# Performance work log

Measured on AMD Instinct MI355X. Metric: run time of the kernel, lower is better.

The kernel has to match this reference:

```python
import jax, jax.numpy as jnp
import numpy as np

N_NODES = 100000
N_EDGES = 1200000
D = 64
NUM_LAYERS = 3
K = 3


def setup_inputs() -> dict:
    key = jax.random.key(0)
    k1, k2, k3, k4 = jax.random.split(key, 4)
    x = jax.random.normal(k1, (N_NODES, D), dtype=jnp.float32)
    edge_index = jax.random.randint(k2, (2, N_EDGES), 0, N_NODES, dtype=jnp.int64)
    # per-layer Chebyshev linear weights [L, K, in, out] and single bias per layer [L, out]
    W = jax.random.normal(k3, (NUM_LAYERS, K, D, D), dtype=jnp.float32) / np.sqrt(D)
    b = jax.random.normal(k4, (NUM_LAYERS, D), dtype=jnp.float32) * 0.01
    return {"x": x, "edge_index": edge_index, "W": W, "b": b}


def _cheb_norm(edge_index, n_nodes):
    # PyG ChebConv.__norm__ with sym normalization, lambda_max=2.0, no edge weights:
    # scaled Laplacian L_hat = -D^{-1/2} A D^{-1/2} (diagonal cancels to 0).
    row, col = edge_index[0], edge_index[1]
    deg = jax.ops.segment_sum(jnp.ones_like(row, dtype=jnp.float32), row,
                              num_segments=n_nodes)
    deg_inv_sqrt = jnp.where(deg > 0, jax.lax.rsqrt(jnp.maximum(deg, 1.0)), 0.0)
    norm = -deg_inv_sqrt[row] * deg_inv_sqrt[col]  # [E]
    return norm


def _propagate(h, src, dst, norm, n_nodes):
    # out[i] = sum_{e: dst_e = i} norm_e * h[src_e]
    msgs = norm[:, None] * h[src]  # [E, D]
    return jax.ops.segment_sum(msgs, dst, num_segments=n_nodes)


def _cheb_conv(h, src, dst, norm, Wl, bl, n_nodes):
    # Tx_0 = h; Tx_1 = L_hat h; Tx_k = 2 L_hat Tx_{k-1} - Tx_{k-2}
    Tx0 = h
    out = Tx0 @ Wl[0]
    Tx1 = _propagate(Tx0, src, dst, norm, n_nodes)
    out = out + Tx1 @ Wl[1]
    for k in range(2, K):
        Tx2 = 2.0 * _propagate(Tx1, src, dst, norm, n_nodes) - Tx0
        out = out + Tx2 @ Wl[k]
        Tx0, Tx1 = Tx1, Tx2
    return out + bl


def reference(x, edge_index, W, b) -> jnp.ndarray:
    n_nodes = x.shape[0]
    src, dst = edge_index[0], edge_index[1]  # flow source_to_target: j=src, i=dst
    norm = _cheb_norm(edge_index, n_nodes)
    # input_dim == hidden_dim -> no input projection; h_prev starts as x
    h_prev = x
    for i in range(NUM_LAYERS):
        inp = x if i == 0 else h_prev
        out = _cheb_conv(inp, src, dst, norm, W[i], b[i], n_nodes)
        if i > 0:
            out = out + h_prev
        h_prev = jax.nn.relu(out)  # dropout identity in eval mode
    return h_prev
```

## Files before the change

### kernel.cpp

```cpp
#include <hip/hip_runtime.h>

#define N_NODES 100000
#define N_EDGES 1200000
#define D 64
#define NUM_LAYERS 3

#define NB 196
#define BSZ 512
#define NPAD (NB * BSZ)
#define CHUNK 4096
#define NCHUNK ((N_EDGES + CHUNK - 1) / CHUNK)
#define ZROW N_NODES
#define BSLACK 3592
#define CAP 8192

typedef unsigned int uint;
typedef unsigned short u16;

using short8 = __attribute__((ext_vector_type(8))) short;
using f32x4  = __attribute__((ext_vector_type(4))) float;

static __device__ __forceinline__ float b2f(u16 u) {
    return __uint_as_float(((uint)u) << 16);
}
static __device__ __forceinline__ u16 f2b(float f) {
    uint u = __float_as_uint(f);
    return (u16)((u + 0x7FFFu + ((u >> 16) & 1u)) >> 16);
}

__global__ __launch_bounds__(256) void part_kernel(const int* __restrict__ src,
        const int* __restrict__ dst, int* __restrict__ cursD, int* __restrict__ cursS,
        int* __restrict__ dstPart, u16* __restrict__ srcPart, int E) {
    __shared__ int eS[CHUNK], eT[CHUNK];
    __shared__ int hD[NB], hS[NB], bD[NB], bS[NB];
    int e0 = blockIdx.x * CHUNK;
    int n = min(CHUNK, E - e0);
    for (int i = threadIdx.x; i < NB; i += 256) { hD[i] = 0; hS[i] = 0; }
    for (int i = threadIdx.x; i < n; i += 256) { eS[i] = src[e0 + i]; eT[i] = dst[e0 + i]; }
    __syncthreads();
    for (int i = threadIdx.x; i < n; i += 256) {
        atomicAdd(&hD[((unsigned)eT[i]) >> 9], 1);
        atomicAdd(&hS[((unsigned)eS[i]) >> 9], 1);
    }
    __syncthreads();
    for (int i = threadIdx.x; i < NB; i += 256) {
        bD[i] = hD[i] ? atomicAdd(&cursD[i], hD[i]) : 0;
        bS[i] = hS[i] ? atomicAdd(&cursS[i], hS[i]) : 0;
        hD[i] = 0; hS[i] = 0;
    }
    __syncthreads();
    for (int i = threadIdx.x; i < n; i += 256) {
        int s = eS[i], t = eT[i];
        int kb = ((unsigned)t) >> 9;
        int pos = bD[kb] + atomicAdd(&hD[kb], 1);
        if (pos < (kb + 1) * CAP) dstPart[pos] = ((t & 511) << 20) | s;
        kb = ((unsigned)s) >> 9;
        pos = bS[kb] + atomicAdd(&hS[kb], 1);
        if (pos < (kb + 1) * CAP) srcPart[pos] = (u16)(s & 511);
    }
}

__global__ __launch_bounds__(256) void csr_kernel(const int* __restrict__ cursD,
        const int* __restrict__ dstPart, int* __restrict__ rowptr,
        int* __restrict__ rowend, int* __restrict__ cv) {
    __shared__ int cnt[BSZ], curs[BSZ], psum[256];
    int b = blockIdx.x, t = threadIdx.x;
    int node0 = b * BSZ;
    int eb = b * CAP;
    int ee = min(cursD[b], (b + 1) * CAP);
    int padbase = eb + b * BSLACK;
    for (int i = t; i < BSZ; i += 256) cnt[i] = 0;
    __syncthreads();
    for (int e = eb + t; e < ee; e += 256)
        atomicAdd(&cnt[((unsigned)dstPart[e]) >> 20], 1);
    __syncthreads();
    int c0 = cnt[2 * t], c1 = cnt[2 * t + 1];
    int p0 = (c0 + 7) & ~7, p1 = (c1 + 7) & ~7;
    psum[t] = p0 + p1;
    __syncthreads();
    for (int off = 1; off < 256; off <<= 1) {
        int u = (t >= off) ? psum[t - off] : 0;
        __syncthreads();
        psum[t] += u;
        __syncthreads();
    }
    int excl = psum[t] - p0 - p1;
    int start0 = padbase + excl;
    int start1 = start0 + p0;
    curs[2 * t] = start0;
    curs[2 * t + 1] = start1;
    int n0 = node0 + 2 * t;
    if (n0 < N_NODES)     { rowptr[n0]     = start0; rowend[n0]     = start0 + p0; }
    if (n0 + 1 < N_NODES) { rowptr[n0 + 1] = start1; rowend[n0 + 1] = start1 + p1; }
    __syncthreads();
    for (int e = eb + t; e < ee; e += 256) {
        int p = dstPart[e];
        int loc = ((unsigned)p) >> 20;
        int pos = atomicAdd(&curs[loc], 1);
        cv[pos] = p & 0xFFFFF;
    }
    __syncthreads();
    for (int q = c0; q < p0; ++q) cv[start0 + q] = ZROW;
    for (int q = c1; q < p1; ++q) cv[start1 + q] = ZROW;
}

__global__ __launch_bounds__(256) void degs_kernel(const int* __restrict__ cursS,
        const u16* __restrict__ srcPart, float* __restrict__ sArr,
        float* __restrict__ rsArr, float* __restrict__ mArr) {
    __shared__ int cnt[BSZ];
    int b = blockIdx.x, t = threadIdx.x;
    int eb = b * CAP;
    int ee = min(cursS[b], (b + 1) * CAP);
    for (int i = t; i < BSZ; i += 256) cnt[i] = 0;
    __syncthreads();
    for (int e = eb + t; e < ee; e += 256)
        atomicAdd(&cnt[srcPart[e]], 1);
    __syncthreads();
    for (int i = t; i < BSZ; i += 256) {
        int node = b * BSZ + i;
        if (node < N_NODES) {
            int d = cnt[i];
            float fd = (float)d;
            sArr[node]  = (d > 0) ? rsqrtf(fd) : 1.0f;
            rsArr[node] = (d > 0) ? sqrtf(fd) : 1.0f;
            mArr[node]  = (d > 0) ? (-1.0f / fd) : 0.0f;
        }
    }
}

__global__ __launch_bounds__(256) void wprep_kernel(const float* __restrict__ W,
        u16* __restrict__ Wb, int* __restrict__ curs2,
        u16* __restrict__ za, u16* __restrict__ zb, u16* __restrict__ zc) {
    if (blockIdx.x == 0) {
        for (int k = threadIdx.x; k < 2 * NB; k += 256)
            curs2[k] = (k < NB ? k : k - NB) * CAP;
        if (threadIdx.x < 192) {
            u16* buf = (threadIdx.x < 64) ? za : (threadIdx.x < 128) ? zb : zc;
            buf[(size_t)ZROW * D + (threadIdx.x & 63)] = 0;
        }
    }
    int i = blockIdx.x * 256 + threadIdx.x;
    if (i >= 72 * 512) return;
    int j = i & 7;
    int lane = (i >> 3) & 63;
    int fid = i >> 9;
    int ni = fid & 1;
    int t = fid >> 1;
    int kt = t % 6;
    int t2 = t / 6;
    int wn = t2 & 1;
    int l = t2 >> 1;
    int k = kt * 32 + (lane >> 4) * 8 + j;
    int col = wn * 32 + ni * 16 + (lane & 15);
    float v = W[((size_t)l * 192 + k) * 64 + col];
    if (l > 0 && k == col) v += 1.0f;
    Wb[i] = f2b(v);
}

__global__ __launch_bounds__(256) void cvt_kernel(const float* __restrict__ x,
        const float* __restrict__ sArr, u16* __restrict__ g0, int nvec) {
    int i = blockIdx.x * blockDim.x + threadIdx.x;
    if (i >= nvec) return;
    float4 v = ((const float4*)x)[i];
    float dv = sArr[i >> 4];
    uint2 b;
    b.x = (uint)f2b(v.x * dv) | ((uint)f2b(v.y * dv) << 16);
    b.y = (uint)f2b(v.z * dv) | ((uint)f2b(v.w * dv) << 16);
    ((uint2*)g0)[i] = b;
}

static __device__ __forceinline__ float gather_one(const int* __restrict__ cv,
        const u16* __restrict__ g, int lane, int p, int pe) {
    float a0 = 0.f, a1 = 0.f, a2 = 0.f, a3 = 0.f,
          a4 = 0.f, a5 = 0.f, a6 = 0.f, a7 = 0.f;
    if (pe - p == 16) {
        int4 c0 = *(const int4*)(cv + p);
        int4 c1 = *(const int4*)(cv + p + 4);
        int4 c2 = *(const int4*)(cv + p + 8);
        int4 c3 = *(const int4*)(cv + p + 12);
        float v0  = b2f(g[(size_t)c0.x * D + lane]);
        float v1  = b2f(g[(size_t)c0.y * D + lane]);
        float v2  = b2f(g[(size_t)c0.z * D + lane]);
        float v3  = b2f(g[(size_t)c0.w * D + lane]);
        float v4  = b2f(g[(size_t)c1.x * D + lane]);
        float v5  = b2f(g[(size_t)c1.y * D + lane]);
        float v6  = b2f(g[(size_t)c1.z * D + lane]);
        float v7  = b2f(g[(size_t)c1.w * D + lane]);
        float v8  = b2f(g[(size_t)c2.x * D + lane]);
        float v9  = b2f(g[(size_t)c2.y * D + lane]);
        float v10 = b2f(g[(size_t)c2.z * D + lane]);
        float v11 = b2f(g[(size_t)c2.w * D + lane]);
        float v12 = b2f(g[(size_t)c3.x * D + lane]);
        float v13 = b2f(g[(size_t)c3.y * D + lane]);
        float v14 = b2f(g[(size_t)c3.z * D + lane]);
        float v15 = b2f(g[(size_t)c3.w * D + lane]);
        a0 = (v0 + v8);  a1 = (v1 + v9);  a2 = (v2 + v10); a3 = (v3 + v11);
        a4 = (v4 + v12); a5 = (v5 + v13); a6 = (v6 + v14); a7 = (v7 + v15);
    } else if (pe > p) {
        int4 ca = *(const int4*)(cv + p);
        int4 cb = *(const int4*)(cv + p + 4);
        for (;;) {
            int np = p + 8;
            bool more = np < pe;
            int4 na, nb;
            if (more) {
                na = *(const int4*)(cv + np);
                nb = *(const int4*)(cv + np + 4);
            }
            a0 += b2f(g[(size_t)ca.x * D + lane]);
            a1 += b2f(g[(size_t)ca.y * D + lane]);
            a2 += b2f(g[(size_t)ca.z * D + lane]);
            a3 += b2f(g[(size_t)ca.w * D + lane]);
            a4 += b2f(g[(size_t)cb.x * D + lane]);
            a5 += b2f(g[(size_t)cb.y * D + lane]);
            a6 += b2f(g[(size_t)cb.z * D + lane]);
            a7 += b2f(g[(size_t)cb.w * D + lane]);
            if (!more) break;
            ca = na; cb = nb; p = np;
        }
    }
    return ((a0 + a1) + (a2 + a3)) + ((a4 + a5) + (a6 + a7));
}

__global__ __launch_bounds__(256) void gather_kernel(const int* __restrict__ rowptr,
        const int* __restrict__ rowend, const int* __restrict__ cv,
        const u16* __restrict__ g, const float* __restrict__ mArr,
        u16* __restrict__ outg, int n) {
    int lane = threadIdx.x & 63;
    int nA = __builtin_amdgcn_readfirstlane((int)(blockIdx.x * 8) + ((threadIdx.x >> 6) << 1));
    if (nA >= n) return;
    const int nB = nA + 1;
    const bool hasB = nB < n;
    int p1 = rowptr[nA], pe1 = rowend[nA];
    int p2 = p1, pe2 = p1;
    if (hasB) { p2 = rowptr[nB]; pe2 = rowend[nB]; }
    float sumA, sumB = 0.0f;

    if ((pe1 - p1 == 16) && (pe2 - p2 == 16)) {
        int4 a0 = *(const int4*)(cv + p1);
        int4 a1 = *(const int4*)(cv + p1 + 4);
        int4 a2 = *(const int4*)(cv + p1 + 8);
        int4 a3 = *(const int4*)(cv + p1 + 12);
        int4 b0 = *(const int4*)(cv + p2);
        int4 b1 = *(const int4*)(cv + p2 + 4);
        int4 b2 = *(const int4*)(cv + p2 + 8);
        int4 b3 = *(const int4*)(cv + p2 + 12);
        float uA0  = b2f(g[(size_t)a0.x * D + lane]);
        float uA1  = b2f(g[(size_t)a0.y * D + lane]);
        float uA2  = b2f(g[(size_t)a0.z * D + lane]);
        float uA3  = b2f(g[(size_t)a0.w * D + lane]);
        float uA4  = b2f(g[(size_t)a1.x * D + lane]);
        float uA5  = b2f(g[(size_t)a1.y * D + lane]);
        float uA6  = b2f(g[(size_t)a1.z * D + lane]);
        float uA7  = b2f(g[(size_t)a1.w * D + lane]);
        float uA8  = b2f(g[(size_t)a2.x * D + lane]);
        float uA9  = b2f(g[(size_t)a2.y * D + lane]);
        float uA10 = b2f(g[(size_t)a2.z * D + lane]);
        float uA11 = b2f(g[(size_t)a2.w * D + lane]);
        float uA12 = b2f(g[(size_t)a3.x * D + lane]);
        float uA13 = b2f(g[(size_t)a3.y * D + lane]);
        float uA14 = b2f(g[(size_t)a3.z * D + lane]);
        float uA15 = b2f(g[(size_t)a3.w * D + lane]);
        float uB0  = b2f(g[(size_t)b0.x * D + lane]);
        float uB1  = b2f(g[(size_t)b0.y * D + lane]);
        float uB2  = b2f(g[(size_t)b0.z * D + lane]);
        float uB3  = b2f(g[(size_t)b0.w * D + lane]);
        float uB4  = b2f(g[(size_t)b1.x * D + lane]);
        float uB5  = b2f(g[(size_t)b1.y * D + lane]);
        float uB6  = b2f(g[(size_t)b1.z * D + lane]);
        float uB7  = b2f(g[(size_t)b1.w * D + lane]);
        float uB8  = b2f(g[(size_t)b2.x * D + lane]);
        float uB9  = b2f(g[(size_t)b2.y * D + lane]);
        float uB10 = b2f(g[(size_t)b2.z * D + lane]);
        float uB11 = b2f(g[(size_t)b2.w * D + lane]);
        float uB12 = b2f(g[(size_t)b3.x * D + lane]);
        float uB13 = b2f(g[(size_t)b3.y * D + lane]);
        float uB14 = b2f(g[(size_t)b3.z * D + lane]);
        float uB15 = b2f(g[(size_t)b3.w * D + lane]);
        sumA = (((uA0 + uA8) + (uA1 + uA9)) + ((uA2 + uA10) + (uA3 + uA11)))
             + (((uA4 + uA12) + (uA5 + uA13)) + ((uA6 + uA14) + (uA7 + uA15)));
        sumB = (((uB0 + uB8) + (uB1 + uB9)) + ((uB2 + uB10) + (uB3 + uB11)))
             + (((uB4 + uB12) + (uB5 + uB13)) + ((uB6 + uB14) + (uB7 + uB15)));
    } else {
        sumA = gather_one(cv, g, lane, p1, pe1);
        sumB = gather_one(cv, g, lane, p2, pe2);
    }

    outg[(size_t)nA * D + lane] = f2b(mArr[nA] * sumA);
    if (hasB)
        outg[(size_t)nB * D + lane] = f2b(mArr[nB] * sumB);
}

__global__ __launch_bounds__(256) void cheb_mfma_kernel(
        const u16* __restrict__ gin, const u16* __restrict__ gt1,
        const u16* __restrict__ gt2, const u16* __restrict__ Wbl,
        const float* __restrict__ bias, const float* __restrict__ rsArr,
        const float* __restrict__ sArr,
        u16* __restrict__ outg, float* __restrict__ outf, int last) {
    const int tid = threadIdx.x;
    const int lane = tid & 63;
    const int w = tid >> 6;
    const int wm = w & 1, wn = w >> 1;
    const int l15 = lane & 15;
    const int l4 = lane >> 4;
    const int koff = l4 * 8;

    const int mbase = blockIdx.x * 64 + wm * 32;
    const int nbase = wn * 32;

    short8 Bf[6][2];
#pragma unroll
    for (int kt = 0; kt < 6; ++kt)
#pragma unroll
        for (int ni = 0; ni < 2; ++ni)
            Bf[kt][ni] = *(const short8*)(Wbl + (size_t)(((wn * 6 + kt) * 2) + ni) * 512 + lane * 8);

    short8 G[2][2], T1[2][2], T2[2][2];
#pragma unroll
    for (int mi = 0; mi < 2; ++mi) {
        int row = mbase + mi * 16 + l15;
#pragma unroll
        for (int half = 0; half < 2; ++half) {
            size_t off = (size_t)row * 64 + half * 32 + koff;
            G[mi][half]  = *(const short8*)(gin + off);
            T1[mi][half] = *(const short8*)(gt1 + off);
            T2[mi][half] = *(const short8*)(gt2 + off);
        }
    }

    float bj0 = bias[nbase + l15];
    float bj1 = bias[nbase + 16 + l15];

    f32x4 acc[2][2];
#pragma unroll
    for (int mi = 0; mi < 2; ++mi)
#pragma unroll
        for (int ni = 0; ni < 2; ++ni)
#pragma unroll
            for (int r = 0; r < 4; ++r) acc[mi][ni][r] = 0.0f;

#pragma unroll
    for (int kt = 0; kt < 6; ++kt) {
        short8 Af[2];
#pragma unroll
        for (int mi = 0; mi < 2; ++mi) {
            short8 a;
            if (kt < 2) {
                a = G[mi][kt];
            } else if (kt < 4) {
                a = T1[mi][kt - 2];
            } else {
                short8 a2 = T2[mi][kt - 4];
                short8 ai = G[mi][kt - 4];
#pragma unroll
                for (int j = 0; j < 8; ++j)
                    a[j] = (short)f2b(fmaf(2.0f, b2f((u16)a2[j]), -b2f((u16)ai[j])));
            }
            Af[mi] = a;
        }
#pragma unroll
        for (int mi = 0; mi < 2; ++mi)
#pragma unroll
            for (int ni = 0; ni < 2; ++ni)
                acc[mi][ni] = __builtin_amdgcn_mfma_f32_16x16x32_bf16(
                    Af[mi], Bf[kt][ni], acc[mi][ni], 0, 0, 0);
    }

    float4 rsv[2], sv[2];
#pragma unroll
    for (int mi = 0; mi < 2; ++mi) {
        rsv[mi] = *(const float4*)(rsArr + mbase + mi * 16 + l4 * 4);
        if (!last) sv[mi] = *(const float4*)(sArr + mbase + mi * 16 + l4 * 4);
    }
#pragma unroll
    for (int mi = 0; mi < 2; ++mi)
#pragma unroll
        for (int r = 0; r < 4; ++r) {
            int node = mbase + mi * 16 + l4 * 4 + r;
            if (node >= N_NODES) continue;
            float rsr = ((const float*)&rsv[mi])[r];
#pragma unroll
            for (int ni = 0; ni < 2; ++ni) {
                int col = nbase + ni * 16 + l15;
                size_t o = (size_t)node * 64 + col;
                float v = fmaf(rsr, acc[mi][ni][r], (ni ? bj1 : bj0));
                v = fmaxf(v, 0.0f);
                if (last) {
                    outf[o] = v;
                } else {
                    float sr = ((const float*)&sv[mi])[r];
                    outg[o] = f2b(v * sr);
                }
            }
        }
}

extern "C" void kernel_launch(void* const* d_in, const int* in_sizes, int n_in,
                              void* d_out, int out_size, void* d_ws, size_t ws_size,
                              hipStream_t stream) {
    const float* x = (const float*)d_in[0];
    const int* ei = (const int*)d_in[1];
    const float* W = (const float*)d_in[2];
    const float* b = (const float*)d_in[3];
    float* out = (float*)d_out;

    const int* src = ei;
    const int* dst = ei + N_EDGES;

    const size_t NDP = (size_t)NPAD * D;
    const size_t CVSZ = (size_t)NB * (CAP + BSLACK) + 64;

    char* w = (char*)d_ws;
    int*   curs2  = (int*)w;        w += (size_t)512 * 4;
    int*   rowptr = (int*)w;        w += (size_t)NPAD * 4;
    int*   rowend = (int*)w;        w += (size_t)NPAD * 4;
    float* sArr   = (float*)w;      w += (size_t)NPAD * 4;
    float* rsArr  = (float*)w;      w += (size_t)NPAD * 4;
    float* mArr   = (float*)w;      w += (size_t)NPAD * 4;
    u16*   Wb     = (u16*)w;        w += (size_t)72 * 512 * 2;
    int*   cv     = (int*)w;        w += ((CVSZ + 63) & ~(size_t)63) * 4;
    u16*   gA     = (u16*)w;        w += NDP * 2;
    u16*   gB     = (u16*)w;        w += NDP * 2;
    u16*   gt1    = (u16*)w;        w += NDP * 2;
    u16*   gt2    = (u16*)w;        w += NDP * 2;
    int*   dstPart = (int*)gt2;
    u16*   srcPart = (u16*)gB;

    int* cursD = curs2;
    int* cursS = curs2 + NB;

    wprep_kernel<<<144, 256, 0, stream>>>(W, Wb, curs2, gA, gB, gt1);
    part_kernel<<<NCHUNK, 256, 0, stream>>>(src, dst, cursD, cursS, dstPart, srcPart, N_EDGES);
    csr_kernel<<<NB, 256, 0, stream>>>(cursD, dstPart, rowptr, rowend, cv);
    degs_kernel<<<NB, 256, 0, stream>>>(cursS, srcPart, sArr, rsArr, mArr);
    cvt_kernel<<<(int)(((size_t)N_NODES * D / 4 + 255) / 256), 256, 0, stream>>>(
        x, sArr, gA, (int)((size_t)N_NODES * D / 4));

    const int gatherBlocks = (N_NODES + 7) / 8;
    const int chebBlocks = NPAD / 64;

    const u16* gin = gA;
    for (int l = 0; l < NUM_LAYERS; ++l) {
        gather_kernel<<<gatherBlocks, 256, 0, stream>>>(rowptr, rowend, cv, gin, mArr, gt1, N_NODES);
        gather_kernel<<<gatherBlocks, 256, 0, stream>>>(rowptr, rowend, cv, gt1, mArr, gt2, N_NODES);

        int last = (l == NUM_LAYERS - 1);
        u16* gout = (l == 0) ? gB : gA;
        cheb_mfma_kernel<<<chebBlocks, 256, 0, stream>>>(
            gin, gt1, gt2, Wb + (size_t)l * 24 * 512, b + (size_t)l * D,
            rsArr, sArr, gout, out, last);
        gin = gout;
    }
}
```

Measured before the change: 287.5 us.

## Fuse second propagation gather into Chebyshev MFMA kernel via shared memory

```diff
diff --git a/kernel.cpp b/kernel.cpp
--- a/kernel.cpp
+++ b/kernel.cpp
@@ -222,20 +222,14 @@
     return ((a0 + a1) + (a2 + a3)) + ((a4 + a5) + (a6 + a7));
 }
 
-__global__ __launch_bounds__(256) void gather_kernel(const int* __restrict__ rowptr,
+static __device__ __forceinline__ void gather_two(const int* __restrict__ rowptr,
         const int* __restrict__ rowend, const int* __restrict__ cv,
-        const u16* __restrict__ g, const float* __restrict__ mArr,
-        u16* __restrict__ outg, int n) {
-    int lane = threadIdx.x & 63;
-    int nA = __builtin_amdgcn_readfirstlane((int)(blockIdx.x * 8) + ((threadIdx.x >> 6) << 1));
-    if (nA >= n) return;
+        const u16* __restrict__ g, int lane, int nA, int n,
+        float& sumA, float& sumB) {
     const int nB = nA + 1;
-    const bool hasB = nB < n;
-    int p1 = rowptr[nA], pe1 = rowend[nA];
-    int p2 = p1, pe2 = p1;
-    if (hasB) { p2 = rowptr[nB]; pe2 = rowend[nB]; }
-    float sumA, sumB = 0.0f;
-
+    int p1 = 0, pe1 = 0, p2 = 0, pe2 = 0;
+    if (nA < n) { p1 = rowptr[nA]; pe1 = rowend[nA]; }
+    if (nB < n) { p2 = rowptr[nB]; pe2 = rowend[nB]; }
     if ((pe1 - p1 == 16) && (pe2 - p2 == 16)) {
         int4 a0 = *(const int4*)(cv + p1);
         int4 a1 = *(const int4*)(cv + p1 + 4);
@@ -285,27 +279,54 @@
         sumA = gather_one(cv, g, lane, p1, pe1);
         sumB = gather_one(cv, g, lane, p2, pe2);
     }
-
+}
+
+__global__ __launch_bounds__(256) void gather_kernel(const int* __restrict__ rowptr,
+        const int* __restrict__ rowend, const int* __restrict__ cv,
+        const u16* __restrict__ g, const float* __restrict__ mArr,
+        u16* __restrict__ outg, int n) {
+    int lane = threadIdx.x & 63;
+    int nA = __builtin_amdgcn_readfirstlane((int)(blockIdx.x * 8) + ((threadIdx.x >> 6) << 1));
+    if (nA >= n) return;
+    float sumA, sumB;
+    gather_two(rowptr, rowend, cv, g, lane, nA, n, sumA, sumB);
     outg[(size_t)nA * D + lane] = f2b(mArr[nA] * sumA);
-    if (hasB)
-        outg[(size_t)nB * D + lane] = f2b(mArr[nB] * sumB);
-}
-
-__global__ __launch_bounds__(256) void cheb_mfma_kernel(
-        const u16* __restrict__ gin, const u16* __restrict__ gt1,
-        const u16* __restrict__ gt2, const u16* __restrict__ Wbl,
-        const float* __restrict__ bias, const float* __restrict__ rsArr,
-        const float* __restrict__ sArr,
-        u16* __restrict__ outg, float* __restrict__ outf, int last) {
+    if (nA + 1 < n)
+        outg[(size_t)(nA + 1) * D + lane] = f2b(mArr[nA + 1] * sumB);
+}
+
+__global__ __launch_bounds__(256) void gather_cheb_kernel(
+        const int* __restrict__ rowptr, const int* __restrict__ rowend,
+        const int* __restrict__ cv, const u16* __restrict__ gt1,
+        const u16* __restrict__ gin, const float* __restrict__ mArr,
+        const u16* __restrict__ Wbl, const float* __restrict__ bias,
+        const float* __restrict__ rsArr, const float* __restrict__ sArr,
+        u16* __restrict__ outg, float* __restrict__ outf, int last, int n) {
+    __shared__ u16 t2l[64][72];
+
     const int tid = threadIdx.x;
     const int lane = tid & 63;
     const int w = tid >> 6;
+    const int base = blockIdx.x * 64;
+
+#pragma unroll 1
+    for (int it = 0; it < 8; ++it) {
+        int nA = __builtin_amdgcn_readfirstlane(base + w * 16 + it * 2);
+        float sumA, sumB;
+        gather_two(rowptr, rowend, cv, gt1, lane, nA, n, sumA, sumB);
+        float mA = (nA < n) ? mArr[nA] : 0.0f;
+        float mB = (nA + 1 < n) ? mArr[nA + 1] : 0.0f;
+        int r = w * 16 + it * 2;
+        t2l[r][lane]     = f2b(mA * sumA);
+        t2l[r + 1][lane] = f2b(mB * sumB);
+    }
+    __syncthreads();
+
     const int wm = w & 1, wn = w >> 1;
     const int l15 = lane & 15;
     const int l4 = lane >> 4;
     const int koff = l4 * 8;
-
-    const int mbase = blockIdx.x * 64 + wm * 32;
+    const int mbase = base + wm * 32;
     const int nbase = wn * 32;
 
     short8 Bf[6][2];
@@ -319,12 +340,13 @@
 #pragma unroll
     for (int mi = 0; mi < 2; ++mi) {
         int row = mbase + mi * 16 + l15;
+        int lrow = wm * 32 + mi * 16 + l15;
 #pragma unroll
         for (int half = 0; half < 2; ++half) {
             size_t off = (size_t)row * 64 + half * 32 + koff;
             G[mi][half]  = *(const short8*)(gin + off);
             T1[mi][half] = *(const short8*)(gt1 + off);
-            T2[mi][half] = *(const short8*)(gt2 + off);
+            T2[mi][half] = *(const short8*)(&t2l[lrow][half * 32 + koff]);
         }
     }
 
@@ -422,8 +444,8 @@
     u16*   gA     = (u16*)w;        w += NDP * 2;
     u16*   gB     = (u16*)w;        w += NDP * 2;
     u16*   gt1    = (u16*)w;        w += NDP * 2;
-    u16*   gt2    = (u16*)w;        w += NDP * 2;
-    int*   dstPart = (int*)gt2;
+    u16*   scratch= (u16*)w;        w += NDP * 2;
+    int*   dstPart = (int*)scratch;
     u16*   srcPart = (u16*)gB;
 
     int* cursD = curs2;
@@ -437,18 +459,18 @@
         x, sArr, gA, (int)((size_t)N_NODES * D / 4));
 
     const int gatherBlocks = (N_NODES + 7) / 8;
-    const int chebBlocks = NPAD / 64;
+    const int fusedBlocks = NPAD / 64;
 
     const u16* gin = gA;
     for (int l = 0; l < NUM_LAYERS; ++l) {
         gather_kernel<<<gatherBlocks, 256, 0, stream>>>(rowptr, rowend, cv, gin, mArr, gt1, N_NODES);
-        gather_kernel<<<gatherBlocks, 256, 0, stream>>>(rowptr, rowend, cv, gt1, mArr, gt2, N_NODES);
 
         int last = (l == NUM_LAYERS - 1);
         u16* gout = (l == 0) ? gB : gA;
-        cheb_mfma_kernel<<<chebBlocks, 256, 0, stream>>>(
-            gin, gt1, gt2, Wb + (size_t)l * 24 * 512, b + (size_t)l * D,
-            rsArr, sArr, gout, out, last);
+        gather_cheb_kernel<<<fusedBlocks, 256, 0, stream>>>(
+            rowptr, rowend, cv, gt1, gin, mArr,
+            Wb + (size_t)l * 24 * 512, b + (size_t)l * D,
+            rsArr, sArr, gout, out, last, N_NODES);
         gin = gout;
     }
 }
```

Result: slower. 306.9 us (+6.8%).
